# Kernel tuning notes

Measured on AMD Instinct MI355X. Metric: run time of the kernel, lower is better.

The kernel has to match this reference:

```python
import jax, jax.numpy as jnp
import numpy as np

# Faithful JAX port of FeatureSimilarity(similarity_type='l2'):
#   -(features[:, None, :] - features[None, :, :]).norm(2, dim=-1)
# Implemented via the algebraically-equal expansion ||x-y||^2 = ||x||^2 + ||y||^2 - 2<x,y>
# to avoid materializing the [N, N, D] broadcast intermediate (32 GB at these sizes).

def setup_inputs() -> dict:
    key = jax.random.key(0)
    features = jax.random.normal(key, (8192, 128), dtype=jnp.float32)  # [N, D]
    return {"features": features}

def reference(features):
    sq = jnp.sum(features * features, axis=-1)                     # [N]
    d2 = sq[:, None] + sq[None, :] - 2.0 * (features @ features.T)  # [N, N]
    d2 = jnp.maximum(d2, 0.0)  # clamp tiny negatives from cancellation
    return -jnp.sqrt(d2)
```

## Files before the change

### kernel.cpp

```cpp
#include <hip/hip_runtime.h>
#include <hip/hip_bf16.h>


typedef __attribute__((ext_vector_type(8))) short short8;
typedef __attribute__((ext_vector_type(4))) float float4v;

#define FS_N 8192
#define FS_D 128

static __device__ __forceinline__ unsigned short f32_to_bf16_rne(float x) {
    unsigned u = __float_as_uint(x);
    u += 0x7FFFu + ((u >> 16) & 1u);
    return (unsigned short)(u >> 16);
}
static __device__ __forceinline__ float bf16_to_f32(unsigned short b) {
    return __uint_as_float(((unsigned)b) << 16);
}

__global__ __launch_bounds__(256) void fs_convert_kernel(
        const float* __restrict__ in, unsigned short* __restrict__ fb,
        float* __restrict__ sq) {
    const int row  = (blockIdx.x << 2) | (threadIdx.x >> 6);
    const int lane = threadIdx.x & 63;
    const float2 v = ((const float2*)(in + row * FS_D))[lane];
    const unsigned short b0 = f32_to_bf16_rne(v.x);
    const unsigned short b1 = f32_to_bf16_rne(v.y);
    ((ushort2*)(fb + row * FS_D))[lane] = make_ushort2(b0, b1);
    const float f0 = bf16_to_f32(b0), f1 = bf16_to_f32(b1);
    float s = f0 * f0 + f1 * f1;
    #pragma unroll
    for (int off = 32; off > 0; off >>= 1) s += __shfl_down(s, off);
    if (lane == 0) sq[row] = s;
}

__global__ __launch_bounds__(256) void fs_gemm_kernel(
        const unsigned short* __restrict__ fb, const float* __restrict__ sq,
        float* __restrict__ out) {
    const int ti   = blockIdx.x;
    const int tj   = blockIdx.y;
    const int wid  = threadIdx.x >> 6;
    const int lane = threadIdx.x & 63;
    const int wm   = wid >> 1, wn = wid & 1;
    const int l15  = lane & 15;
    const int quad = lane >> 4;

    const int arow = ti * 128 + wm * 64;
    const int brow = tj * 128 + wn * 64;

    float4v acc[4][4];
    #pragma unroll
    for (int m = 0; m < 4; ++m)
        #pragma unroll
        for (int n = 0; n < 4; ++n)
            acc[m][n] = (float4v){0.f, 0.f, 0.f, 0.f};

    #pragma unroll
    for (int ks = 0; ks < 4; ++ks) {
        const int kofs = ks * 32 + quad * 8;
        short8 a[4], b[4];
        #pragma unroll
        for (int m = 0; m < 4; ++m)
            a[m] = *(const short8*)(fb + (arow + m * 16 + l15) * FS_D + kofs);
        #pragma unroll
        for (int n = 0; n < 4; ++n)
            b[n] = *(const short8*)(fb + (brow + n * 16 + l15) * FS_D + kofs);
        #pragma unroll
        for (int m = 0; m < 4; ++m)
            #pragma unroll
            for (int n = 0; n < 4; ++n)
                acc[m][n] = __builtin_amdgcn_mfma_f32_16x16x32_bf16(
                    a[m], b[n], acc[m][n], 0, 0, 0);
    }

    #pragma unroll
    for (int m = 0; m < 4; ++m) {
        const float4v sqr = *(const float4v*)(sq + arow + m * 16 + quad * 4);
        #pragma unroll
        for (int n = 0; n < 4; ++n) {
            const int   col = brow + n * 16 + l15;
            const float sqc = sq[col];
            #pragma unroll
            for (int r = 0; r < 4; ++r) {
                const int row = arow + m * 16 + quad * 4 + r;
                float d2 = sqr[r] + sqc - 2.0f * acc[m][n][r];
                d2 = fmaxf(d2, 0.0f);
                out[row * FS_N + col] = -__builtin_sqrtf(d2);
            }
        }
    }
}

extern "C" void kernel_launch(void* const* d_in, const int* in_sizes, int n_in,
                              void* d_out, int out_size, void* d_ws, size_t ws_size,
                              hipStream_t stream) {
    const float* features = (const float*)d_in[0];
    float*       out      = (float*)d_out;

    unsigned short* fb = (unsigned short*)d_ws;
    float*          sq = (float*)((char*)d_ws + (size_t)FS_N * FS_D * sizeof(unsigned short));

    fs_convert_kernel<<<FS_N / 4, 256, 0, stream>>>(features, fb, sq);

    dim3 grid(FS_N / 128, FS_N / 128);
    fs_gemm_kernel<<<grid, 256, 0, stream>>>(fb, sq, out);
}
```

Baseline: 293.8 us.

## Pre-swizzle bf16 operands into MFMA fragment order and store output via symmetric transpose

```diff
diff --git a/kernel.cpp b/kernel.cpp
--- a/kernel.cpp
+++ b/kernel.cpp
@@ -18,23 +18,43 @@
 }
 
 __global__ __launch_bounds__(256) void fs_convert_kernel(
-        const float* __restrict__ in, unsigned short* __restrict__ fb,
+        const float* __restrict__ in, unsigned short* __restrict__ fbT,
         float* __restrict__ sq) {
-    const int row  = (blockIdx.x << 2) | (threadIdx.x >> 6);
-    const int lane = threadIdx.x & 63;
-    const float2 v = ((const float2*)(in + row * FS_D))[lane];
-    const unsigned short b0 = f32_to_bf16_rne(v.x);
-    const unsigned short b1 = f32_to_bf16_rne(v.y);
-    ((ushort2*)(fb + row * FS_D))[lane] = make_ushort2(b0, b1);
-    const float f0 = bf16_to_f32(b0), f1 = bf16_to_f32(b1);
-    float s = f0 * f0 + f1 * f1;
+    const int rt = blockIdx.x;
+    const int t  = threadIdx.x;
+    const int rl = t >> 4;
+    const int g  = t & 15;
+    const int row = rt * 16 + rl;
+
+    const float4* src = (const float4*)(in + row * FS_D + g * 8);
+    const float4 v0 = src[0];
+    const float4 v1 = src[1];
+
+    short8 packed;
+    float s = 0.0f;
+    {
+        const float vv[8] = {v0.x, v0.y, v0.z, v0.w, v1.x, v1.y, v1.z, v1.w};
+        #pragma unroll
+        for (int e = 0; e < 8; ++e) {
+            const unsigned short b = f32_to_bf16_rne(vv[e]);
+            packed[e] = (short)b;
+            const float f = bf16_to_f32(b);
+            s += f * f;
+        }
+    }
+
+    const int ks   = g >> 2;
+    const int quad = g & 3;
+    short8* dst = (short8*)(fbT + (((size_t)(rt * 4 + ks) * 64) + quad * 16 + rl) * 8);
+    *dst = packed;
+
     #pragma unroll
-    for (int off = 32; off > 0; off >>= 1) s += __shfl_down(s, off);
-    if (lane == 0) sq[row] = s;
+    for (int off = 8; off > 0; off >>= 1) s += __shfl_xor(s, off);
+    if (g == 0) sq[row] = s;
 }
 
 __global__ __launch_bounds__(256) void fs_gemm_kernel(
-        const unsigned short* __restrict__ fb, const float* __restrict__ sq,
+        const unsigned short* __restrict__ fbT, const float* __restrict__ sq,
         float* __restrict__ out) {
     const int ti   = blockIdx.x;
     const int tj   = blockIdx.y;
@@ -47,6 +67,9 @@
     const int arow = ti * 128 + wm * 64;
     const int brow = tj * 128 + wn * 64;
 
+    const int rta = ti * 8 + wm * 4;
+    const int rtb = tj * 8 + wn * 4;
+
     float4v acc[4][4];
     #pragma unroll
     for (int m = 0; m < 4; ++m)
@@ -56,14 +79,13 @@
 
     #pragma unroll
     for (int ks = 0; ks < 4; ++ks) {
-        const int kofs = ks * 32 + quad * 8;
         short8 a[4], b[4];
         #pragma unroll
         for (int m = 0; m < 4; ++m)
-            a[m] = *(const short8*)(fb + (arow + m * 16 + l15) * FS_D + kofs);
+            a[m] = *(const short8*)(fbT + (size_t)((rta + m) * 4 + ks) * 512 + lane * 8);
         #pragma unroll
         for (int n = 0; n < 4; ++n)
-            b[n] = *(const short8*)(fb + (brow + n * 16 + l15) * FS_D + kofs);
+            b[n] = *(const short8*)(fbT + (size_t)((rtb + n) * 4 + ks) * 512 + lane * 8);
         #pragma unroll
         for (int m = 0; m < 4; ++m)
             #pragma unroll
@@ -73,19 +95,22 @@
     }
 
     #pragma unroll
-    for (int m = 0; m < 4; ++m) {
-        const float4v sqr = *(const float4v*)(sq + arow + m * 16 + quad * 4);
+    for (int n = 0; n < 4; ++n) {
+        const int   col = brow + n * 16 + l15;
+        const float sqc = sq[col];
+        float* outcol = out + (size_t)col * FS_N;
         #pragma unroll
-        for (int n = 0; n < 4; ++n) {
-            const int   col = brow + n * 16 + l15;
-            const float sqc = sq[col];
+        for (int m = 0; m < 4; ++m) {
+            const int rbase = arow + m * 16 + quad * 4;
+            const float4v sqr = *(const float4v*)(sq + rbase);
+            float4v o;
             #pragma unroll
             for (int r = 0; r < 4; ++r) {
-                const int row = arow + m * 16 + quad * 4 + r;
                 float d2 = sqr[r] + sqc - 2.0f * acc[m][n][r];
                 d2 = fmaxf(d2, 0.0f);
-                out[row * FS_N + col] = -__builtin_sqrtf(d2);
+                o[r] = -__builtin_sqrtf(d2);
             }
+            *(float4v*)(outcol + rbase) = o;
         }
     }
 }
@@ -96,11 +121,11 @@
     const float* features = (const float*)d_in[0];
     float*       out      = (float*)d_out;
 
-    unsigned short* fb = (unsigned short*)d_ws;
-    float*          sq = (float*)((char*)d_ws + (size_t)FS_N * FS_D * sizeof(unsigned short));
+    unsigned short* fbT = (unsigned short*)d_ws;
+    float*          sq  = (float*)((char*)d_ws + (size_t)FS_N * FS_D * sizeof(unsigned short));
 
-    fs_convert_kernel<<<FS_N / 4, 256, 0, stream>>>(features, fb, sq);
+    fs_convert_kernel<<<FS_N / 16, 256, 0, stream>>>(features, fbT, sq);
 
     dim3 grid(FS_N / 128, FS_N / 128);
-    fs_gemm_kernel<<<grid, 256, 0, stream>>>(fb, sq, out);
+    fs_gemm_kernel<<<grid, 256, 0, stream>>>(fbT, sq, out);
 }
```

Result: faster. 279.1 us (-5.0%).
